# Kernel optimization log

Hardware: AMD Instinct MI355X
Metric: run time of the kernel (lower is better)

The kernel has to match this reference:

```python
import jax, jax.numpy as jnp
import numpy as np

BS, CIN, COUT, OUT_DIM, S, S0 = 64, 128, 128, 1024, 2, 1
BLK = S * (S0 + 1)  # 4
D = OUT_DIM * BLK   # 4096


def setup_inputs() -> dict:
    key = jax.random.key(0)
    kx, kw = jax.random.split(key)
    x = jax.random.normal(kx, (BS, CIN, D), dtype=jnp.float32)
    weight = jax.random.normal(kw, (COUT, CIN, D), dtype=jnp.float32)
    return {"x": x, "weight": weight}


def reference(x, weight):
    # Equivalent to: (x[:, None] * weight).reshape(bs, cout, cin, out_dim, blk).sum((-1, -3)) / sqrt(cin)
    bs, cin, d = x.shape
    cout = weight.shape[0]
    blk = BLK
    xr = x.reshape(bs, cin, d // blk, blk)          # (bs, cin, out_dim, blk)
    wr = weight.reshape(cout, cin, d // blk, blk)   # (cout, cin, out_dim, blk)
    # Blocked locally-connected contraction over (cin, blk), fused -- never
    # materializes the (bs, cout, cin, d) broadcast intermediate.
    out = jnp.einsum('bink,oink->bon', xr, wr)
    return out / jnp.sqrt(jnp.asarray(cin, dtype=x.dtype))
```

## Files before the change

### kernel.cpp

```cpp
#include <hip/hip_runtime.h>


#define CIN  128
#define COUT 128
#define ODIM 1024
#define DDIM 4096
#define CI   8
#define NCH  16
#define RS   512
#define R4B  (4u * CIN * DDIM * 4u)
#define CHB  ((unsigned)(CI * DDIM * 4))

typedef short bf16x8 __attribute__((ext_vector_type(8)));
typedef short s16x4  __attribute__((ext_vector_type(4)));
typedef float f32x4  __attribute__((ext_vector_type(4)));

static __device__ __forceinline__ unsigned short f2bf(float f) {
    unsigned int u = __float_as_uint(f);
    u += 0x7fffu + ((u >> 16) & 1u);
    return (unsigned short)(u >> 16);
}
static __device__ __forceinline__ s16x4 cvt4(float4 v) {
    s16x4 s;
    s[0] = (short)f2bf(v.x); s[1] = (short)f2bf(v.y);
    s[2] = (short)f2bf(v.z); s[3] = (short)f2bf(v.w);
    return s;
}

__global__ __launch_bounds__(512, 4)
void nolc_kernel(const float* __restrict__ xg,
                 const float* __restrict__ wg,
                 float* __restrict__ outg) {
    __shared__ short lds[64 * RS];

    const int bid  = blockIdx.x;
    const int gidx = (bid & 7) * 64 + (bid >> 3);
    const int ng   = gidx >> 3;
    const int bq   = (gidx >> 2) & 1;
    const int oq   = gidx & 3;

    const int t    = threadIdx.x;
    const int lane = t & 63;
    const int wave = t >> 6;

    const int sn = t & 15;
    const int si = (t >> 4) & 7;
    const int rl = t >> 7;

    const unsigned xoff =
        ((unsigned)((bq * 32 + rl) * CIN + si) * DDIM + (unsigned)(ng * 64 + sn * 4)) * 4u;
    const unsigned woff =
        ((unsigned)((oq * 32 + rl) * CIN + si) * DDIM + (unsigned)(ng * 64 + sn * 4)) * 4u;

    const int bt  = wave & 1;
    const int ot  = (wave >> 1) & 1;
    const int nh  = wave >> 2;
    const int r16 = lane & 15;
    const int kg  = lane >> 4;

    f32x4 acc[8];
#pragma unroll
    for (int n = 0; n < 8; ++n) acc[n] = (f32x4){0.f, 0.f, 0.f, 0.f};

    float4 fx0, fx1, fx2, fx3, fx4, fx5, fx6, fx7;
    float4 fw0, fw1, fw2, fw3, fw4, fw5, fw6, fw7;

#define GLD(dst, off, base) \
    asm volatile("global_load_dwordx4 %0, %1, %2" : "=v"(dst) : "v"(off), "s"(base))

#define ISSUE_X(c) do { unsigned _o = xoff + (unsigned)(c) * CHB;            \
    GLD(fx0, _o,           xg); GLD(fx1, _o + 1u*R4B, xg);                   \
    GLD(fx2, _o + 2u*R4B,  xg); GLD(fx3, _o + 3u*R4B, xg);                   \
    GLD(fx4, _o + 4u*R4B,  xg); GLD(fx5, _o + 5u*R4B, xg);                   \
    GLD(fx6, _o + 6u*R4B,  xg); GLD(fx7, _o + 7u*R4B, xg); } while (0)

#define ISSUE_W(c) do { unsigned _o = woff + (unsigned)(c) * CHB;            \
    GLD(fw0, _o,           wg); GLD(fw1, _o + 1u*R4B, wg);                   \
    GLD(fw2, _o + 2u*R4B,  wg); GLD(fw3, _o + 3u*R4B, wg);                   \
    GLD(fw4, _o + 4u*R4B,  wg); GLD(fw5, _o + 5u*R4B, wg);                   \
    GLD(fw6, _o + 6u*R4B,  wg); GLD(fw7, _o + 7u*R4B, wg); } while (0)

#define STROW(v, it, rbase) do {                                             \
    const int _row = (rbase) + (it) * 4 + rl;                                \
    *reinterpret_cast<s16x4*>(                                               \
        &lds[_row * RS + si * 64 + ((sn ^ (_row & 15)) << 2)]) = cvt4(v);    \
    } while (0)

#define STX() do { STROW(fx0,0,0); STROW(fx1,1,0); STROW(fx2,2,0); STROW(fx3,3,0); \
                   STROW(fx4,4,0); STROW(fx5,5,0); STROW(fx6,6,0); STROW(fx7,7,0); } while (0)
#define STW() do { STROW(fw0,0,32); STROW(fw1,1,32); STROW(fw2,2,32); STROW(fw3,3,32); \
                   STROW(fw4,4,32); STROW(fw5,5,32); STROW(fw6,6,32); STROW(fw7,7,32); } while (0)

#define VMW8() do { asm volatile("s_waitcnt vmcnt(8)" ::: "memory");         \
                    __builtin_amdgcn_sched_barrier(0); } while (0)
#define VMW0() do { asm volatile("s_waitcnt vmcnt(0)" ::: "memory");         \
                    __builtin_amdgcn_sched_barrier(0); } while (0)

    const int xbase = (bt * 16 + r16) * RS;
    const int wbase = (32 + ot * 16 + r16) * RS;

    ISSUE_X(0);
    ISSUE_W(0);

#pragma unroll 1
    for (int c = 0; c < NCH; ++c) {
        VMW8();
        STX();
        if (c + 1 < NCH) ISSUE_X(c + 1);

        if (c + 1 < NCH) { VMW8(); }
        else             { VMW0(); }
        STW();
        if (c + 1 < NCH) ISSUE_W(c + 1);

        asm volatile("s_waitcnt lgkmcnt(0)" ::: "memory");
        __builtin_amdgcn_sched_barrier(0);
        __builtin_amdgcn_s_barrier();

#pragma unroll
        for (int nn = 0; nn < 8; ++nn) {
            const int n  = nh * 8 + nn;
            const int so = (n ^ r16) << 2;
            s16x4 a0 = *reinterpret_cast<const s16x4*>(&lds[xbase + (kg * 2) * 64 + so]);
            s16x4 a1 = *reinterpret_cast<const s16x4*>(&lds[xbase + (kg * 2 + 1) * 64 + so]);
            s16x4 b0 = *reinterpret_cast<const s16x4*>(&lds[wbase + (kg * 2) * 64 + so]);
            s16x4 b1 = *reinterpret_cast<const s16x4*>(&lds[wbase + (kg * 2 + 1) * 64 + so]);
            bf16x8 A = __builtin_shufflevector(a0, a1, 0, 1, 2, 3, 4, 5, 6, 7);
            bf16x8 B = __builtin_shufflevector(b0, b1, 0, 1, 2, 3, 4, 5, 6, 7);
            acc[nn] = __builtin_amdgcn_mfma_f32_16x16x32_bf16(A, B, acc[nn], 0, 0, 0);
        }
        if (c + 1 < NCH) __builtin_amdgcn_s_barrier();
    }

    const float scale = 0.08838834764831845f;
    const int o = oq * 32 + ot * 16 + r16;
#pragma unroll
    for (int r = 0; r < 4; ++r) {
        const int b = bq * 32 + bt * 16 + kg * 4 + r;
        float* op = outg + ((size_t)b * COUT + o) * ODIM + ng * 16 + nh * 8;
        float4 v0, v1;
        v0.x = acc[0][r] * scale; v0.y = acc[1][r] * scale;
        v0.z = acc[2][r] * scale; v0.w = acc[3][r] * scale;
        v1.x = acc[4][r] * scale; v1.y = acc[5][r] * scale;
        v1.z = acc[6][r] * scale; v1.w = acc[7][r] * scale;
        *reinterpret_cast<float4*>(op)     = v0;
        *reinterpret_cast<float4*>(op + 4) = v1;
    }
}

extern "C" void kernel_launch(void* const* d_in, const int* in_sizes, int n_in,
                              void* d_out, int out_size, void* d_ws, size_t ws_size,
                              hipStream_t stream) {
    const float* x = (const float*)d_in[0];
    const float* w = (const float*)d_in[1];
    float* out = (float*)d_out;
    nolc_kernel<<<dim3(512), dim3(512), 0, stream>>>(x, w, out);
}
```

Before: 140.2 us.

## Pre-pack inputs to bf16 blocked layout, then run a larger-tile GEMM kernel

Result: slower. 198.9 us (+41.9%).

```diff
diff --git a/kernel.cpp b/kernel.cpp
--- a/kernel.cpp
+++ b/kernel.cpp
@@ -5,13 +5,14 @@
 #define COUT 128
 #define ODIM 1024
 #define DDIM 4096
-#define CI   8
-#define NCH  16
-#define RS   512
-#define R4B  (4u * CIN * DDIM * 4u)
-#define CHB  ((unsigned)(CI * DDIM * 4))
+#define NGS   128
+#define NGSTR 262144
+#define XP_SHORTS (NGS * NGSTR)
+#define WP_SHORTS (2 * NGS * NGSTR)
+#define WS_NEED   ((size_t)(XP_SHORTS + WP_SHORTS) * 2)
 
 typedef short bf16x8 __attribute__((ext_vector_type(8)));
+typedef short s16x8  __attribute__((ext_vector_type(8)));
 typedef short s16x4  __attribute__((ext_vector_type(4)));
 typedef float f32x4  __attribute__((ext_vector_type(4)));
 
@@ -27,100 +28,196 @@
     return s;
 }
 
+#define GLD(dst, off, base) \
+    asm volatile("global_load_dwordx4 %0, %1, %2" : "=v"(dst) : "v"(off), "s"(base))
+
 __global__ __launch_bounds__(512, 4)
-void nolc_kernel(const float* __restrict__ xg,
-                 const float* __restrict__ wg,
-                 float* __restrict__ outg) {
+void pack_kernel(const float* __restrict__ xg, const float* __restrict__ wg,
+                 short* __restrict__ Xp, short* __restrict__ Wp) {
+    const int W    = blockIdx.x * 8 + (threadIdx.x >> 6);
+    const int lane = threadIdx.x & 63;
+
+    const float* src;
+    short* dst0;
+    int ngstride;
+    if (W < 8192) {
+        src = xg + (size_t)W * DDIM;
+        dst0 = Xp + (W & 127) * 2048 + (W >> 7) * 32;
+        ngstride = NGSTR;
+    } else {
+        const int W2 = W - 8192;
+        const int o = W2 >> 7, i = W2 & 127;
+        src = wg + (size_t)W2 * DDIM;
+        dst0 = Wp + (o >> 6) * NGSTR + i * 2048 + (o & 63) * 32;
+        ngstride = 2 * NGSTR;
+    }
+    const float4* s4 = reinterpret_cast<const float4*>(src);
+#pragma unroll
+    for (int rep = 0; rep < 16; ++rep) {
+        const int d4 = rep * 64 + lane;
+        float4 v = s4[d4];
+        const int ng = d4 >> 3, n = d4 & 7;
+        *reinterpret_cast<s16x4*>(dst0 + (size_t)ng * ngstride + n * 4) = cvt4(v);
+    }
+}
+
+__global__ __launch_bounds__(512, 4)
+void gemm2_kernel(const short* __restrict__ Xp, const short* __restrict__ Wp,
+                  float* __restrict__ outg) {
+    __shared__ short xs[64 * 256];
+    __shared__ short ws2[64 * 256];
+
+    const int bid  = blockIdx.x;
+    const int gidx = (bid & 7) * 32 + (bid >> 3);
+    const int ng   = gidx >> 1;
+    const int oh   = gidx & 1;
+
+    const int t    = threadIdx.x;
+    const int lane = t & 63;
+    const int wave = t >> 6;
+    const int bt   = wave & 3;
+    const int ot   = wave >> 2;
+    const int r16  = lane & 15;
+    const int kg   = lane >> 4;
+
+    const short* xb = Xp + (size_t)ng * NGSTR;
+    const short* wb = Wp + (size_t)(ng * 2 + oh) * NGSTR;
+
+    const int srow = (t >> 2) & 63;
+    const int sn0  = (t & 3) * 2;
+    const int sib  = t >> 8;
+    const int sb7  = srow & 7;
+    const int ss0  = sn0 ^ sb7;
+    const unsigned tb = (unsigned)t * 16u;
+
+    f32x4 acc[2][8];
+#pragma unroll
+    for (int j = 0; j < 2; ++j)
+#pragma unroll
+        for (int n = 0; n < 8; ++n) acc[j][n] = (f32x4){0.f, 0.f, 0.f, 0.f};
+
+    s16x8 px0, px1, px2, px3, pw0, pw1, pw2, pw3;
+
+#define ISSUE_X(c) do { unsigned _o = tb + (unsigned)(c) * 32768u;           \
+    GLD(px0, _o, xb); GLD(px1, _o + 8192u, xb);                              \
+    GLD(px2, _o + 16384u, xb); GLD(px3, _o + 24576u, xb); } while (0)
+#define ISSUE_W(c) do { unsigned _o = tb + (unsigned)(c) * 32768u;           \
+    GLD(pw0, _o, wb); GLD(pw1, _o + 8192u, wb);                              \
+    GLD(pw2, _o + 16384u, wb); GLD(pw3, _o + 24576u, wb); } while (0)
+
+#define ST1(arr, v, it) do {                                                 \
+    const int _a = srow * 256 + ((it) * 2 + sib) * 32 + ss0 * 4;             \
+    const int _b = srow * 256 + ((it) * 2 + sib) * 32 + (ss0 ^ 1) * 4;       \
+    *reinterpret_cast<s16x4*>(&arr[_a]) =                                    \
+        __builtin_shufflevector(v, v, 0, 1, 2, 3);                           \
+    *reinterpret_cast<s16x4*>(&arr[_b]) =                                    \
+        __builtin_shufflevector(v, v, 4, 5, 6, 7);                           \
+    } while (0)
+#define STX() do { ST1(xs, px0, 0); ST1(xs, px1, 1); ST1(xs, px2, 2); ST1(xs, px3, 3); } while (0)
+#define STW() do { ST1(ws2, pw0, 0); ST1(ws2, pw1, 1); ST1(ws2, pw2, 2); ST1(ws2, pw3, 3); } while (0)
+
+#define VMW4() do { asm volatile("s_waitcnt vmcnt(4)" ::: "memory");         \
+                    __builtin_amdgcn_sched_barrier(0); } while (0)
+#define VMW0() do { asm volatile("s_waitcnt vmcnt(0)" ::: "memory");         \
+                    __builtin_amdgcn_sched_barrier(0); } while (0)
+
+    const int xrow  = (bt * 16 + r16) * 256;
+    const int orow0 = (ot * 32 + r16) * 256;
+    const int orow1 = (ot * 32 + 16 + r16) * 256;
+    const int rb7   = r16 & 7;
+    const int kgo   = kg * 64;
+
+    ISSUE_X(0); ISSUE_W(0);
+#pragma unroll 1
+    for (int c = 0; c < 16; ++c) {
+        VMW4();
+        STX();
+        if (c + 1 < 16) ISSUE_X(c + 1);
+        if (c + 1 < 16) { VMW4(); }
+        else            { VMW0(); }
+        STW();
+        if (c + 1 < 16) ISSUE_W(c + 1);
+        asm volatile("s_waitcnt lgkmcnt(0)" ::: "memory");
+        __builtin_amdgcn_sched_barrier(0);
+        __builtin_amdgcn_s_barrier();
+
+#pragma unroll
+        for (int n = 0; n < 8; ++n) {
+            const int so = (n ^ rb7) * 4;
+            s16x4 a0 = *reinterpret_cast<const s16x4*>(&xs[xrow + kgo + so]);
+            s16x4 a1 = *reinterpret_cast<const s16x4*>(&xs[xrow + kgo + 32 + so]);
+            s16x4 b0 = *reinterpret_cast<const s16x4*>(&ws2[orow0 + kgo + so]);
+            s16x4 b1 = *reinterpret_cast<const s16x4*>(&ws2[orow0 + kgo + 32 + so]);
+            s16x4 c0 = *reinterpret_cast<const s16x4*>(&ws2[orow1 + kgo + so]);
+            s16x4 c1 = *reinterpret_cast<const s16x4*>(&ws2[orow1 + kgo + 32 + so]);
+            bf16x8 A  = __builtin_shufflevector(a0, a1, 0, 1, 2, 3, 4, 5, 6, 7);
+            bf16x8 B0 = __builtin_shufflevector(b0, b1, 0, 1, 2, 3, 4, 5, 6, 7);
+            bf16x8 B1 = __builtin_shufflevector(c0, c1, 0, 1, 2, 3, 4, 5, 6, 7);
+            acc[0][n] = __builtin_amdgcn_mfma_f32_16x16x32_bf16(A, B0, acc[0][n], 0, 0, 0);
+            acc[1][n] = __builtin_amdgcn_mfma_f32_16x16x32_bf16(A, B1, acc[1][n], 0, 0, 0);
+        }
+        if (c + 1 < 16) __builtin_amdgcn_s_barrier();
+    }
+
+    const float scale = 0.08838834764831845f;
+#pragma unroll
+    for (int osub = 0; osub < 2; ++osub) {
+        const int o = oh * 64 + ot * 32 + osub * 16 + r16;
+#pragma unroll
+        for (int r = 0; r < 4; ++r) {
+            const int b = bt * 16 + kg * 4 + r;
+            float* op = outg + ((size_t)b * COUT + o) * ODIM + ng * 8;
+            float4 v0, v1;
+            v0.x = acc[osub][0][r] * scale; v0.y = acc[osub][1][r] * scale;
+            v0.z = acc[osub][2][r] * scale; v0.w = acc[osub][3][r] * scale;
+            v1.x = acc[osub][4][r] * scale; v1.y = acc[osub][5][r] * scale;
+            v1.z = acc[osub][6][r] * scale; v1.w = acc[osub][7][r] * scale;
+            *reinterpret_cast<float4*>(op)     = v0;
+            *reinterpret_cast<float4*>(op + 4) = v1;
+        }
+    }
+}
+
+#define RS 512
+__global__ __launch_bounds__(512, 4)
+void nolc_fallback(const float* __restrict__ xg, const float* __restrict__ wg,
+                   float* __restrict__ outg) {
     __shared__ short lds[64 * RS];
-
     const int bid  = blockIdx.x;
     const int gidx = (bid & 7) * 64 + (bid >> 3);
     const int ng   = gidx >> 3;
     const int bq   = (gidx >> 2) & 1;
     const int oq   = gidx & 3;
-
-    const int t    = threadIdx.x;
-    const int lane = t & 63;
-    const int wave = t >> 6;
-
-    const int sn = t & 15;
-    const int si = (t >> 4) & 7;
-    const int rl = t >> 7;
-
-    const unsigned xoff =
-        ((unsigned)((bq * 32 + rl) * CIN + si) * DDIM + (unsigned)(ng * 64 + sn * 4)) * 4u;
-    const unsigned woff =
-        ((unsigned)((oq * 32 + rl) * CIN + si) * DDIM + (unsigned)(ng * 64 + sn * 4)) * 4u;
-
-    const int bt  = wave & 1;
-    const int ot  = (wave >> 1) & 1;
-    const int nh  = wave >> 2;
-    const int r16 = lane & 15;
-    const int kg  = lane >> 4;
-
+    const int t = threadIdx.x, lane = t & 63, wave = t >> 6;
+    const int sn = t & 15, si = (t >> 4) & 7, rl = t >> 7;
+    const float* px = xg + ((size_t)(bq * 32 + rl) * CIN + si) * DDIM + ng * 64 + sn * 4;
+    const float* pw = wg + ((size_t)(oq * 32 + rl) * CIN + si) * DDIM + ng * 64 + sn * 4;
+    const size_t R4 = (size_t)4 * CIN * DDIM, CH = (size_t)8 * DDIM;
+    const int bt = wave & 1, ot = (wave >> 1) & 1, nh = wave >> 2;
+    const int r16 = lane & 15, kg = lane >> 4;
     f32x4 acc[8];
 #pragma unroll
     for (int n = 0; n < 8; ++n) acc[n] = (f32x4){0.f, 0.f, 0.f, 0.f};
-
-    float4 fx0, fx1, fx2, fx3, fx4, fx5, fx6, fx7;
-    float4 fw0, fw1, fw2, fw3, fw4, fw5, fw6, fw7;
-
-#define GLD(dst, off, base) \
-    asm volatile("global_load_dwordx4 %0, %1, %2" : "=v"(dst) : "v"(off), "s"(base))
-
-#define ISSUE_X(c) do { unsigned _o = xoff + (unsigned)(c) * CHB;            \
-    GLD(fx0, _o,           xg); GLD(fx1, _o + 1u*R4B, xg);                   \
-    GLD(fx2, _o + 2u*R4B,  xg); GLD(fx3, _o + 3u*R4B, xg);                   \
-    GLD(fx4, _o + 4u*R4B,  xg); GLD(fx5, _o + 5u*R4B, xg);                   \
-    GLD(fx6, _o + 6u*R4B,  xg); GLD(fx7, _o + 7u*R4B, xg); } while (0)
-
-#define ISSUE_W(c) do { unsigned _o = woff + (unsigned)(c) * CHB;            \
-    GLD(fw0, _o,           wg); GLD(fw1, _o + 1u*R4B, wg);                   \
-    GLD(fw2, _o + 2u*R4B,  wg); GLD(fw3, _o + 3u*R4B, wg);                   \
-    GLD(fw4, _o + 4u*R4B,  wg); GLD(fw5, _o + 5u*R4B, wg);                   \
-    GLD(fw6, _o + 6u*R4B,  wg); GLD(fw7, _o + 7u*R4B, wg); } while (0)
-
-#define STROW(v, it, rbase) do {                                             \
-    const int _row = (rbase) + (it) * 4 + rl;                                \
-    *reinterpret_cast<s16x4*>(                                               \
-        &lds[_row * RS + si * 64 + ((sn ^ (_row & 15)) << 2)]) = cvt4(v);    \
-    } while (0)
-
-#define STX() do { STROW(fx0,0,0); STROW(fx1,1,0); STROW(fx2,2,0); STROW(fx3,3,0); \
-                   STROW(fx4,4,0); STROW(fx5,5,0); STROW(fx6,6,0); STROW(fx7,7,0); } while (0)
-#define STW() do { STROW(fw0,0,32); STROW(fw1,1,32); STROW(fw2,2,32); STROW(fw3,3,32); \
-                   STROW(fw4,4,32); STROW(fw5,5,32); STROW(fw6,6,32); STROW(fw7,7,32); } while (0)
-
-#define VMW8() do { asm volatile("s_waitcnt vmcnt(8)" ::: "memory");         \
-                    __builtin_amdgcn_sched_barrier(0); } while (0)
-#define VMW0() do { asm volatile("s_waitcnt vmcnt(0)" ::: "memory");         \
-                    __builtin_amdgcn_sched_barrier(0); } while (0)
-
-    const int xbase = (bt * 16 + r16) * RS;
-    const int wbase = (32 + ot * 16 + r16) * RS;
-
-    ISSUE_X(0);
-    ISSUE_W(0);
-
+    const int xbase = (bt * 16 + r16) * RS, wbase = (32 + ot * 16 + r16) * RS;
 #pragma unroll 1
-    for (int c = 0; c < NCH; ++c) {
-        VMW8();
-        STX();
-        if (c + 1 < NCH) ISSUE_X(c + 1);
-
-        if (c + 1 < NCH) { VMW8(); }
-        else             { VMW0(); }
-        STW();
-        if (c + 1 < NCH) ISSUE_W(c + 1);
-
-        asm volatile("s_waitcnt lgkmcnt(0)" ::: "memory");
-        __builtin_amdgcn_sched_barrier(0);
-        __builtin_amdgcn_s_barrier();
-
+    for (int c = 0; c < 16; ++c) {
+        float4 rx[8], rw[8];
+#pragma unroll
+        for (int it = 0; it < 8; ++it) {
+            rx[it] = *reinterpret_cast<const float4*>(px + c * CH + it * R4);
+            rw[it] = *reinterpret_cast<const float4*>(pw + c * CH + it * R4);
+        }
+#pragma unroll
+        for (int it = 0; it < 8; ++it) {
+            const int row = it * 4 + rl;
+            *reinterpret_cast<s16x4*>(&lds[row * RS + si * 64 + ((sn ^ (row & 15)) << 2)]) = cvt4(rx[it]);
+            const int row2 = 32 + it * 4 + rl;
+            *reinterpret_cast<s16x4*>(&lds[row2 * RS + si * 64 + ((sn ^ (row2 & 15)) << 2)]) = cvt4(rw[it]);
+        }
+        __syncthreads();
 #pragma unroll
         for (int nn = 0; nn < 8; ++nn) {
-            const int n  = nh * 8 + nn;
-            const int so = (n ^ r16) << 2;
+            const int n = nh * 8 + nn, so = (n ^ r16) << 2;
             s16x4 a0 = *reinterpret_cast<const s16x4*>(&lds[xbase + (kg * 2) * 64 + so]);
             s16x4 a1 = *reinterpret_cast<const s16x4*>(&lds[xbase + (kg * 2 + 1) * 64 + so]);
             s16x4 b0 = *reinterpret_cast<const s16x4*>(&lds[wbase + (kg * 2) * 64 + so]);
@@ -129,9 +226,8 @@
             bf16x8 B = __builtin_shufflevector(b0, b1, 0, 1, 2, 3, 4, 5, 6, 7);
             acc[nn] = __builtin_amdgcn_mfma_f32_16x16x32_bf16(A, B, acc[nn], 0, 0, 0);
         }
-        if (c + 1 < NCH) __builtin_amdgcn_s_barrier();
-    }
-
+        if (c + 1 < 16) __syncthreads();
+    }
     const float scale = 0.08838834764831845f;
     const int o = oq * 32 + ot * 16 + r16;
 #pragma unroll
@@ -143,7 +239,7 @@
         v0.z = acc[2][r] * scale; v0.w = acc[3][r] * scale;
         v1.x = acc[4][r] * scale; v1.y = acc[5][r] * scale;
         v1.z = acc[6][r] * scale; v1.w = acc[7][r] * scale;
-        *reinterpret_cast<float4*>(op)     = v0;
+        *reinterpret_cast<float4*>(op) = v0;
         *reinterpret_cast<float4*>(op + 4) = v1;
     }
 }
@@ -154,5 +250,12 @@
     const float* x = (const float*)d_in[0];
     const float* w = (const float*)d_in[1];
     float* out = (float*)d_out;
-    nolc_kernel<<<dim3(512), dim3(512), 0, stream>>>(x, w, out);
-}
+    if (ws_size >= WS_NEED) {
+        short* Xp = (short*)d_ws;
+        short* Wp = Xp + XP_SHORTS;
+        pack_kernel<<<dim3(3072), dim3(512), 0, stream>>>(x, w, Xp, Wp);
+        gemm2_kernel<<<dim3(256), dim3(512), 0, stream>>>(Xp, Wp, out);
+    } else {
+        nolc_fallback<<<dim3(512), dim3(512), 0, stream>>>(x, w, out);
+    }
+}
```
